# Optimization experiments

Hardware: AMD Instinct MI355X
Metric: run time of the kernel (lower is better)

## Reference

```python
import jax, jax.numpy as jnp
import numpy as np

DIM = 1024
HID = 2048
E = 8
K = 2
INV_SQRT2 = 1.0 / 1.41421356237


def setup_inputs() -> dict:
    key = jax.random.key(0)
    ks = jax.random.split(key, 10)
    s = lambda fan_in: 1.0 / np.sqrt(fan_in)
    return {
        "x": jax.random.normal(ks[0], (4, 2048, DIM), dtype=jnp.float32),
        "gate_w": jax.random.uniform(ks[1], (DIM, E), jnp.float32, -s(DIM), s(DIM)),
        "gate_b": jnp.zeros((E,), jnp.float32),
        "w1": jax.random.uniform(ks[2], (E, DIM, HID), jnp.float32, -s(DIM), s(DIM)),
        "b1": jnp.zeros((E, HID), jnp.float32),
        "w2": jax.random.uniform(ks[3], (E, DIM, HID), jnp.float32, -s(DIM), s(DIM)),
        "b2": jnp.zeros((E, HID), jnp.float32),
        "w3": jax.random.uniform(ks[4], (E, HID, DIM), jnp.float32, -s(HID), s(HID)),
        "b3": jnp.zeros((E, DIM), jnp.float32),
    }


def reference(x, gate_w, gate_b, w1, b1, w2, b2, w3, b3):
    # Gating
    logits = jnp.einsum("bsd,de->bse", x, gate_w) + gate_b          # [b,s,E]
    scores = jax.nn.softmax(logits, axis=-1)
    topk_scores, topk_idx = jax.lax.top_k(scores, K)                  # [b,s,K]

    # Load-balance (entropy) loss over mean expert usage
    usage = scores.mean(axis=(0, 1))                                   # [E]
    lb_loss = -(usage * jnp.log(usage + 1e-9)).sum()

    # Per-token combine weight for each expert: score if expert in top-k else 0
    onehot = jax.nn.one_hot(topk_idx, E, dtype=x.dtype)               # [b,s,K,E]
    comb = (topk_scores[..., None] * onehot).sum(axis=2)              # [b,s,E]

    # SwiGLU experts (batched over E via einsum)
    h = jnp.einsum("bsd,edh->ebsh", x, w1) + b1[:, None, None, :]
    g = jax.nn.silu(jnp.einsum("bsd,edh->ebsh", x, w2) + b2[:, None, None, :])
    eo = jnp.einsum("ebsh,ehd->ebsd", h * g, w3) + b3[:, None, None, :]
    eo = eo * INV_SQRT2

    # Weighted combine (zero weight where expert not selected)
    out = jnp.einsum("ebsd,bse->bsd", eo, comb)
    return out, lb_loss
```

## Files before the change

kernel.cpp:

```cpp
#include <hip/hip_runtime.h>
#include <cstdio>

#define NTOK 8192
#define DIM 1024
#define HID 2048
#define NE 8
#define NPAIR (NTOK * 2)

typedef __attribute__((ext_vector_type(8))) short bf16x8;
typedef __attribute__((ext_vector_type(4))) float f32x4;

typedef const __attribute__((address_space(1))) void* gas_ptr;
typedef __attribute__((address_space(3))) void* las_ptr;

__device__ __forceinline__ void async16(const void* g, void* s) {
  __builtin_amdgcn_global_load_lds((gas_ptr)g, (las_ptr)s, 16, 0, 0);
}

__device__ __forceinline__ unsigned short f2bf(float f) {
  unsigned int u = __float_as_uint(f);
  u = (u + 0x7fff + ((u >> 16) & 1)) >> 16;
  return (unsigned short)u;
}

__device__ __forceinline__ float bf2f(unsigned short u) {
  return __uint_as_float((unsigned int)u << 16);
}


#define S_BARRIER __builtin_amdgcn_s_barrier()
#define VM_WAIT(N) asm volatile("s_waitcnt vmcnt(" #N ")" ::: "memory")
#define LGKM0 asm volatile("s_waitcnt lgkmcnt(0)" ::: "memory")
#define CFENCE asm volatile("" ::: "memory")

__global__ __launch_bounds__(256) void prep_kernel(
    const float* __restrict__ w1, const float* __restrict__ w2,
    const float* __restrict__ w3, unsigned short* __restrict__ w1bt,
    unsigned short* __restrict__ w2bt, unsigned short* __restrict__ w3bt) {
  const int z = blockIdx.y;
  const int m = z >> 3, e = z & 7;
  int R, C;
  const float* in;
  unsigned short* outp;
  if (m == 0)      { R = DIM; C = HID; in = w1; outp = w1bt; }
  else if (m == 1) { R = DIM; C = HID; in = w2; outp = w2bt; }
  else             { R = HID; C = DIM; in = w3; outp = w3bt; }
  in += (size_t)e * DIM * HID;
  outp += (size_t)e * DIM * HID;

  const int tilesx = C >> 5;
  const int c0 = (blockIdx.x % tilesx) * 32;
  const int r0 = (blockIdx.x / tilesx) * 32;

  __shared__ float tile[32][33];
  const int c = threadIdx.x & 31, rr = threadIdx.x >> 5;
#pragma unroll
  for (int i = 0; i < 4; i++) {
    const int r = rr + i * 8;
    tile[r][c] = in[(size_t)(r0 + r) * C + c0 + c];
  }
  __syncthreads();
#pragma unroll
  for (int i = 0; i < 4; i++) {
    const int cc2 = rr + i * 8;
    outp[(size_t)(c0 + cc2) * R + r0 + c] = f2bf(tile[c][cc2]);
  }
}

__global__ __launch_bounds__(256) void gate_kernel(
    const float* __restrict__ x, const float* __restrict__ gw,
    const float* __restrict__ gb, unsigned short* __restrict__ xb,
    float* __restrict__ scores, int* __restrict__ route_e,
    float* __restrict__ route_w) {
  __shared__ float sgwT[NE][DIM];
  const int tid = threadIdx.x;
#pragma unroll
  for (int i = 0; i < 8; i++) {
    const int j = i * 256 + tid;
    const float4 v = ((const float4*)gw)[j];
    const int d = j >> 1, e0 = (j & 1) * 4;
    sgwT[e0 + 0][d] = v.x; sgwT[e0 + 1][d] = v.y;
    sgwT[e0 + 2][d] = v.z; sgwT[e0 + 3][d] = v.w;
  }
  __syncthreads();

  const int wv = tid >> 6, lane = tid & 63;
  const int t = blockIdx.x * 4 + wv;
  float acc[NE] = {0.f, 0.f, 0.f, 0.f, 0.f, 0.f, 0.f, 0.f};
  const float4* x4 = (const float4*)(x + (size_t)t * DIM);
#pragma unroll
  for (int i = 0; i < 4; i++) {
    const float4 xv = x4[i * 64 + lane];
    const int d4 = i * 64 + lane;
    ushort4 xbv;
    xbv.x = f2bf(xv.x); xbv.y = f2bf(xv.y);
    xbv.z = f2bf(xv.z); xbv.w = f2bf(xv.w);
    *(ushort4*)(xb + (size_t)t * DIM + d4 * 4) = xbv;
#pragma unroll
    for (int e = 0; e < NE; e++) {
      const float4 wv4 = *(const float4*)&sgwT[e][d4 * 4];
      acc[e] += xv.x * wv4.x + xv.y * wv4.y + xv.z * wv4.z + xv.w * wv4.w;
    }
  }
#pragma unroll
  for (int e = 0; e < NE; e++)
#pragma unroll
    for (int s = 32; s; s >>= 1) acc[e] += __shfl_xor(acc[e], s, 64);

  if (lane == 0) {
    float l[NE], m = -1e30f;
#pragma unroll
    for (int e = 0; e < NE; e++) { l[e] = acc[e] + gb[e]; m = fmaxf(m, l[e]); }
    float p[NE], sum = 0.f;
#pragma unroll
    for (int e = 0; e < NE; e++) { p[e] = __expf(l[e] - m); sum += p[e]; }
    const float inv = 1.f / sum;
    float s[NE];
#pragma unroll
    for (int e = 0; e < NE; e++) { s[e] = p[e] * inv; scores[t * NE + e] = s[e]; }
    int i1 = 0;
    for (int e = 1; e < NE; e++) if (s[e] > s[i1]) i1 = e;
    int i2 = -1;
    for (int e = 0; e < NE; e++) {
      if (e == i1) continue;
      if (i2 < 0 || s[e] > s[i2]) i2 = e;
    }
    route_e[t * 2] = i1; route_e[t * 2 + 1] = i2;
    route_w[t * 2] = s[i1]; route_w[t * 2 + 1] = s[i2];
  }
}

__global__ void finalize_kernel(const float* __restrict__ scores,
                                const int* __restrict__ route_e,
                                int* __restrict__ ctrl,
                                float* __restrict__ out_lb) {
  __shared__ float red[1024];
  __shared__ int hist[NE];
  const int tid = threadIdx.x;
  if (tid < NE) hist[tid] = 0;
  const int e = tid & 7, row = tid >> 3;
  float s = 0.f;
  for (int i = 0; i < 64; i++) s += scores[(size_t)(row + i * 128) * NE + e];
  red[tid] = s;
  __syncthreads();
#pragma unroll
  for (int i = 0; i < 16; i++)
    atomicAdd(&hist[route_e[i * 1024 + tid]], 1);
  for (int st = 512; st >= 8; st >>= 1) {
    __syncthreads();
    if (tid < st) red[tid] += red[tid + st];
  }
  __syncthreads();
  if (tid == 0) {
    float lb = 0.f;
    for (int ee = 0; ee < NE; ee++) {
      const float u = red[ee] * (1.f / 8192.f);
      lb -= u * __logf(u + 1e-9f);
    }
    *out_lb = lb;
    int o = 0;
    for (int ee = 0; ee < NE; ee++) {
      ctrl[ee] = hist[ee];
      ctrl[8 + ee] = o;
      ctrl[17 + ee] = o;
      o += hist[ee];
    }
    ctrl[16] = o;
  }
}

__global__ void scatter_kernel(const int* __restrict__ route_e,
                               const float* __restrict__ route_w,
                               int* __restrict__ ctrl,
                               int* __restrict__ tok_list,
                               float* __restrict__ pair_w,
                               int* __restrict__ pair_pos) {
  const int t = blockIdx.x * 256 + threadIdx.x;
  if (t >= NTOK) return;
#pragma unroll
  for (int k = 0; k < 2; k++) {
    const int e = route_e[t * 2 + k];
    const int p = atomicAdd(&ctrl[17 + e], 1);
    tok_list[p] = t;
    pair_w[p] = route_w[t * 2 + k] * 0.70710678118654752f;
    pair_pos[t * 2 + k] = p;
  }
}

__global__ __launch_bounds__(512) void stage1_kernel(
    const unsigned short* __restrict__ xb, const unsigned short* __restrict__ w1bt,
    const unsigned short* __restrict__ w2bt, const float* __restrict__ b1,
    const float* __restrict__ b2, const int* __restrict__ tok_list,
    const int* __restrict__ ctrl, unsigned short* __restrict__ act) {
  const int e = blockIdx.z;
  const int cnt = ctrl[e];
  const int ytile = blockIdx.y;
  if (ytile * 256 >= cnt) return;
  const int off = ctrl[8 + e];
  const int rows = min(256, cnt - ytile * 256);
  const int h0 = blockIdx.x * 128;

  __shared__ unsigned short sX[4][256 * 32];
  __shared__ unsigned short sW1[4][128 * 32];
  __shared__ unsigned short sW2[4][128 * 32];

  const int tid = threadIdx.x;
  const int wv = tid >> 6, lane = tid & 63;

  const int cl = ((tid & 3) ^ ((tid >> 3) & 3)) * 8;

  const unsigned short* w1p = w1bt + (size_t)e * HID * DIM + (size_t)h0 * DIM;
  const unsigned short* w2p = w2bt + (size_t)e * HID * DIM + (size_t)h0 * DIM;
  const unsigned short* gx0 =
      xb + (size_t)tok_list[off + ytile * 256 + min(tid >> 2, rows - 1)] * DIM + cl;
  const unsigned short* gx1 =
      xb + (size_t)tok_list[off + ytile * 256 + min(128 + (tid >> 2), rows - 1)] * DIM + cl;
  const unsigned short* gw1 = w1p + (size_t)(tid >> 2) * DIM + cl;
  const unsigned short* gw2 = w2p + (size_t)(tid >> 2) * DIM + cl;

  f32x4 ah[8][2], ag[8][2];
#pragma unroll
  for (int i = 0; i < 8; i++)
#pragma unroll
    for (int j = 0; j < 2; j++) {
      ah[i][j] = (f32x4){0.f, 0.f, 0.f, 0.f};
      ag[i][j] = (f32x4){0.f, 0.f, 0.f, 0.f};
    }

  const int wr = wv >> 2, wc = wv & 3;
  const int l15 = lane & 15, q = lane >> 4;
  const int pch = (q ^ ((l15 >> 1) & 3)) * 8;

#define S1_STAGE(B)                                   \
  do {                                                \
    async16(gx0, sX[B] + (wv * 64) * 8);              \
    async16(gx1, sX[B] + (512 + wv * 64) * 8);        \
    async16(gw1, sW1[B] + (wv * 64) * 8);             \
    async16(gw2, sW2[B] + (wv * 64) * 8);             \
    gx0 += 32; gx1 += 32; gw1 += 32; gw2 += 32;       \
  } while (0)

  S1_STAGE(0); S1_STAGE(1); S1_STAGE(2);
  VM_WAIT(8);
  S_BARRIER;
  CFENCE;

  const int NT = DIM / 32;
  for (int t = 0; t < NT; t++) {
    const int cur = t & 3;
    bf16x8 bx[8], a1[2], a2[2];
    {
      const unsigned short* xs = sX[cur];
      const unsigned short* w1s = sW1[cur];
      const unsigned short* w2s = sW2[cur];
#pragma unroll
      for (int i = 0; i < 8; i++)
        bx[i] = *(const bf16x8*)(xs + (wr * 128 + i * 16 + l15) * 32 + pch);
#pragma unroll
      for (int j = 0; j < 2; j++) {
        a1[j] = *(const bf16x8*)(w1s + (wc * 32 + j * 16 + l15) * 32 + pch);
        a2[j] = *(const bf16x8*)(w2s + (wc * 32 + j * 16 + l15) * 32 + pch);
      }
    }
    if (t < NT - 3) {
      const int nb = (t + 3) & 3;
      S1_STAGE(nb);
    }
    S_BARRIER;
    LGKM0;
    __builtin_amdgcn_sched_barrier(0);
    __builtin_amdgcn_s_setprio(1);
#pragma unroll
    for (int i = 0; i < 8; i++) {
      ah[i][0] = __builtin_amdgcn_mfma_f32_16x16x32_bf16(a1[0], bx[i], ah[i][0], 0, 0, 0);
      ag[i][0] = __builtin_amdgcn_mfma_f32_16x16x32_bf16(a2[0], bx[i], ag[i][0], 0, 0, 0);
      ah[i][1] = __builtin_amdgcn_mfma_f32_16x16x32_bf16(a1[1], bx[i], ah[i][1], 0, 0, 0);
      ag[i][1] = __builtin_amdgcn_mfma_f32_16x16x32_bf16(a2[1], bx[i], ag[i][1], 0, 0, 0);
    }
    __builtin_amdgcn_s_setprio(0);
    if (t < NT - 3) VM_WAIT(8);
    else if (t == NT - 3) VM_WAIT(4);
    else if (t == NT - 2) VM_WAIT(0);
    CFENCE;
    S_BARRIER;
  }
#undef S1_STAGE

  f32x4 b1v[2], b2v[2];
#pragma unroll
  for (int j = 0; j < 2; j++) {
    const int hc = h0 + wc * 32 + j * 16 + q * 4;
    b1v[j] = *(const f32x4*)(b1 + e * HID + hc);
    b2v[j] = *(const f32x4*)(b2 + e * HID + hc);
  }
#pragma unroll
  for (int i = 0; i < 8; i++) {
    const int trow = wr * 128 + i * 16 + l15;
    if (trow < rows) {
      const size_t gp = (size_t)(off + ytile * 256 + trow) * HID;
#pragma unroll
      for (int j = 0; j < 2; j++) {
        const int hc = h0 + wc * 32 + j * 16 + q * 4;
        ushort4 o;
        {
          const float hh = ah[i][j][0] + b1v[j][0];
          const float gg = ag[i][j][0] + b2v[j][0];
          o.x = f2bf(hh * (gg / (1.f + __expf(-gg))));
        }
        {
          const float hh = ah[i][j][1] + b1v[j][1];
          const float gg = ag[i][j][1] + b2v[j][1];
          o.y = f2bf(hh * (gg / (1.f + __expf(-gg))));
        }
        {
          const float hh = ah[i][j][2] + b1v[j][2];
          const float gg = ag[i][j][2] + b2v[j][2];
          o.z = f2bf(hh * (gg / (1.f + __expf(-gg))));
        }
        {
          const float hh = ah[i][j][3] + b1v[j][3];
          const float gg = ag[i][j][3] + b2v[j][3];
          o.w = f2bf(hh * (gg / (1.f + __expf(-gg))));
        }
        *(ushort4*)(act + gp + hc) = o;
      }
    }
  }
}

__global__ __launch_bounds__(512) void stage2s_kernel(
    const unsigned short* __restrict__ act, const unsigned short* __restrict__ w3bt,
    const float* __restrict__ b3, const float* __restrict__ pair_w,
    const int* __restrict__ ctrl, unsigned short* __restrict__ pair_out) {
  const int e = blockIdx.z;
  const int cnt = ctrl[e];
  const int ytile = blockIdx.y;
  if (ytile * 256 >= cnt) return;
  const int off = ctrl[8 + e];
  const int rows = min(256, cnt - ytile * 256);
  const int d0 = blockIdx.x * 256;
  const int rbase = off + ytile * 256;

  __shared__ unsigned short sA[4][256 * 32];
  __shared__ unsigned short sW[4][256 * 32];

  const int tid = threadIdx.x;
  const int wv = tid >> 6, lane = tid & 63;
  const int cl = ((tid & 3) ^ ((tid >> 3) & 3)) * 8;

  const unsigned short* w3p = w3bt + (size_t)e * DIM * HID + (size_t)d0 * HID;
  const unsigned short* ga0 =
      act + (size_t)(rbase + min(tid >> 2, rows - 1)) * HID + cl;
  const unsigned short* ga1 =
      act + (size_t)(rbase + min(128 + (tid >> 2), rows - 1)) * HID + cl;
  const unsigned short* gw0 = w3p + (size_t)(tid >> 2) * HID + cl;
  const unsigned short* gw1 = w3p + (size_t)(128 + (tid >> 2)) * HID + cl;

  f32x4 acc[8][4];
#pragma unroll
  for (int i = 0; i < 8; i++)
#pragma unroll
    for (int j = 0; j < 4; j++) acc[i][j] = (f32x4){0.f, 0.f, 0.f, 0.f};

  const int wr = wv >> 2, wc = wv & 3;
  const int l15 = lane & 15, q = lane >> 4;
  const int pch = (q ^ ((l15 >> 1) & 3)) * 8;

#define S2_STAGE(B)                                   \
  do {                                                \
    async16(ga0, sA[B] + (wv * 64) * 8);              \
    async16(ga1, sA[B] + (512 + wv * 64) * 8);        \
    async16(gw0, sW[B] + (wv * 64) * 8);              \
    async16(gw1, sW[B] + (512 + wv * 64) * 8);        \
    ga0 += 32; ga1 += 32; gw0 += 32; gw1 += 32;       \
  } while (0)

  S2_STAGE(0); S2_STAGE(1); S2_STAGE(2);
  VM_WAIT(8);
  S_BARRIER;
  CFENCE;

  const int NT = HID / 32;
  for (int t = 0; t < NT; t++) {
    const int cur = t & 3;
    bf16x8 af[8], bf[4];
    {
      const unsigned short* as = sA[cur];
      const unsigned short* ws = sW[cur];
#pragma unroll
      for (int i = 0; i < 8; i++)
        af[i] = *(const bf16x8*)(as + (wr * 128 + i * 16 + l15) * 32 + pch);
#pragma unroll
      for (int j = 0; j < 4; j++)
        bf[j] = *(const bf16x8*)(ws + (wc * 64 + j * 16 + l15) * 32 + pch);
    }
    if (t < NT - 3) {
      const int nb = (t + 3) & 3;
      S2_STAGE(nb);
    }
    S_BARRIER;
    LGKM0;
    __builtin_amdgcn_sched_barrier(0);
    __builtin_amdgcn_s_setprio(1);
#pragma unroll
    for (int i = 0; i < 8; i++)
#pragma unroll
      for (int j = 0; j < 4; j++)
        acc[i][j] =
            __builtin_amdgcn_mfma_f32_16x16x32_bf16(af[i], bf[j], acc[i][j], 0, 0, 0);
    __builtin_amdgcn_s_setprio(0);
    if (t < NT - 3) VM_WAIT(8);
    else if (t == NT - 3) VM_WAIT(4);
    else if (t == NT - 2) VM_WAIT(0);
    CFENCE;
    S_BARRIER;
  }
#undef S2_STAGE

#pragma unroll
  for (int i = 0; i < 8; i++)
#pragma unroll
    for (int rg = 0; rg < 4; rg++) {
      const int row = wr * 128 + i * 16 + q * 4 + rg;
      if (row < rows) {
        const int pr = rbase + row;
        const float wt = pair_w[pr];
#pragma unroll
        for (int j = 0; j < 4; j++) {
          const int dcol = d0 + wc * 64 + j * 16 + l15;
          pair_out[(size_t)pr * DIM + dcol] = f2bf((acc[i][j][rg] + b3[e * DIM + dcol]) * wt);
        }
      }
    }
}

__global__ __launch_bounds__(512) void stage2a_kernel(
    const unsigned short* __restrict__ act, const unsigned short* __restrict__ w3bt,
    const float* __restrict__ b3, const int* __restrict__ tok_list,
    const float* __restrict__ pair_w, const int* __restrict__ ctrl,
    float* __restrict__ out) {
  const int e = blockIdx.z;
  const int cnt = ctrl[e];
  const int ytile = blockIdx.y;
  if (ytile * 256 >= cnt) return;
  const int off = ctrl[8 + e];
  const int rows = min(256, cnt - ytile * 256);
  const int d0 = blockIdx.x * 256;
  const int rbase = off + ytile * 256;

  __shared__ unsigned short sA[4][256 * 32];
  __shared__ unsigned short sW[4][256 * 32];

  const int tid = threadIdx.x;
  const int wv = tid >> 6, lane = tid & 63;
  const int cl = ((tid & 3) ^ ((tid >> 3) & 3)) * 8;

  const unsigned short* w3p = w3bt + (size_t)e * DIM * HID + (size_t)d0 * HID;
  const unsigned short* ga0 =
      act + (size_t)(rbase + min(tid >> 2, rows - 1)) * HID + cl;
  const unsigned short* ga1 =
      act + (size_t)(rbase + min(128 + (tid >> 2), rows - 1)) * HID + cl;
  const unsigned short* gw0 = w3p + (size_t)(tid >> 2) * HID + cl;
  const unsigned short* gw1 = w3p + (size_t)(128 + (tid >> 2)) * HID + cl;

  f32x4 acc[8][4];
#pragma unroll
  for (int i = 0; i < 8; i++)
#pragma unroll
    for (int j = 0; j < 4; j++) acc[i][j] = (f32x4){0.f, 0.f, 0.f, 0.f};

  const int wr = wv >> 2, wc = wv & 3;
  const int l15 = lane & 15, q = lane >> 4;
  const int pch = (q ^ ((l15 >> 1) & 3)) * 8;

#define S2A_STAGE(B)                                  \
  do {                                                \
    async16(ga0, sA[B] + (wv * 64) * 8);              \
    async16(ga1, sA[B] + (512 + wv * 64) * 8);        \
    async16(gw0, sW[B] + (wv * 64) * 8);              \
    async16(gw1, sW[B] + (512 + wv * 64) * 8);        \
    ga0 += 32; ga1 += 32; gw0 += 32; gw1 += 32;       \
  } while (0)

  S2A_STAGE(0); S2A_STAGE(1); S2A_STAGE(2);
  VM_WAIT(8);
  S_BARRIER;
  CFENCE;

  const int NT = HID / 32;
  for (int t = 0; t < NT; t++) {
    const int cur = t & 3;
    bf16x8 af[8], bf[4];
    {
      const unsigned short* as = sA[cur];
      const unsigned short* ws = sW[cur];
#pragma unroll
      for (int i = 0; i < 8; i++)
        af[i] = *(const bf16x8*)(as + (wr * 128 + i * 16 + l15) * 32 + pch);
#pragma unroll
      for (int j = 0; j < 4; j++)
        bf[j] = *(const bf16x8*)(ws + (wc * 64 + j * 16 + l15) * 32 + pch);
    }
    if (t < NT - 3) {
      const int nb = (t + 3) & 3;
      S2A_STAGE(nb);
    }
    S_BARRIER;
    LGKM0;
    __builtin_amdgcn_sched_barrier(0);
    __builtin_amdgcn_s_setprio(1);
#pragma unroll
    for (int i = 0; i < 8; i++)
#pragma unroll
      for (int j = 0; j < 4; j++)
        acc[i][j] =
            __builtin_amdgcn_mfma_f32_16x16x32_bf16(af[i], bf[j], acc[i][j], 0, 0, 0);
    __builtin_amdgcn_s_setprio(0);
    if (t < NT - 3) VM_WAIT(8);
    else if (t == NT - 3) VM_WAIT(4);
    else if (t == NT - 2) VM_WAIT(0);
    CFENCE;
    S_BARRIER;
  }
#undef S2A_STAGE

#pragma unroll
  for (int i = 0; i < 8; i++)
#pragma unroll
    for (int rg = 0; rg < 4; rg++) {
      const int row = wr * 128 + i * 16 + q * 4 + rg;
      if (row < rows) {
        const int pr = rbase + row;
        const int tok = tok_list[pr];
        const float wt = pair_w[pr];
#pragma unroll
        for (int j = 0; j < 4; j++) {
          const int dcol = d0 + wc * 64 + j * 16 + l15;
          atomicAdd(out + (size_t)tok * DIM + dcol, (acc[i][j][rg] + b3[e * DIM + dcol]) * wt);
        }
      }
    }
}

__global__ __launch_bounds__(256) void combine_kernel(
    const unsigned short* __restrict__ pair_out, const int* __restrict__ pair_pos,
    float* __restrict__ out) {
  const int t = blockIdx.x;
  const int d = threadIdx.x * 4;
  const int p0 = pair_pos[t * 2], p1 = pair_pos[t * 2 + 1];
  const ushort4 a = *(const ushort4*)(pair_out + (size_t)p0 * DIM + d);
  const ushort4 b = *(const ushort4*)(pair_out + (size_t)p1 * DIM + d);
  float4 r;
  r.x = bf2f(a.x) + bf2f(b.x);
  r.y = bf2f(a.y) + bf2f(b.y);
  r.z = bf2f(a.z) + bf2f(b.z);
  r.w = bf2f(a.w) + bf2f(b.w);
  *(float4*)(out + (size_t)t * DIM + d) = r;
}

static const size_t SZ_XB  = (size_t)NTOK * DIM * 2;
static const size_t SZ_W   = (size_t)NE * DIM * HID * 2;
static const size_t SZ_ACT = (size_t)NPAIR * HID * 2;
static const size_t OFF_XB  = 0;
static const size_t OFF_W1  = OFF_XB + SZ_XB;
static const size_t OFF_W2  = OFF_W1 + SZ_W;
static const size_t OFF_W3  = OFF_W2 + SZ_W;
static const size_t OFF_ACT = OFF_W3 + SZ_W;
static const size_t OFF_SC  = OFF_ACT + SZ_ACT;
static const size_t OFF_RE  = OFF_SC + (size_t)NTOK * NE * 4;
static const size_t OFF_RW  = OFF_RE + (size_t)NPAIR * 4;
static const size_t OFF_TL  = OFF_RW + (size_t)NPAIR * 4;
static const size_t OFF_PW  = OFF_TL + (size_t)NPAIR * 4;
static const size_t OFF_PP  = OFF_PW + (size_t)NPAIR * 4;
static const size_t OFF_CT  = OFF_PP + (size_t)NPAIR * 4;
static const size_t WS_BASE = OFF_CT + 128;
static const size_t OFF_PO  = WS_BASE;
static const size_t WS_FULL = OFF_PO + (size_t)NPAIR * DIM * 2;

extern "C" void kernel_launch(void* const* d_in, const int* in_sizes, int n_in,
                              void* d_out, int out_size, void* d_ws, size_t ws_size,
                              hipStream_t stream) {
  const float* x      = (const float*)d_in[0];
  const float* gate_w = (const float*)d_in[1];
  const float* gate_b = (const float*)d_in[2];
  const float* w1     = (const float*)d_in[3];
  const float* b1     = (const float*)d_in[4];
  const float* w2     = (const float*)d_in[5];
  const float* b2     = (const float*)d_in[6];
  const float* w3     = (const float*)d_in[7];
  const float* b3     = (const float*)d_in[8];
  float* out = (float*)d_out;

  if (ws_size < WS_BASE) {
    fprintf(stderr, "kernel_launch: ws_size %zu < needed %zu\n", ws_size, WS_BASE);
    return;
  }
  const bool store_path = (ws_size >= WS_FULL);

  char* ws = (char*)d_ws;
  unsigned short* xb   = (unsigned short*)(ws + OFF_XB);
  unsigned short* w1bt = (unsigned short*)(ws + OFF_W1);
  unsigned short* w2bt = (unsigned short*)(ws + OFF_W2);
  unsigned short* w3bt = (unsigned short*)(ws + OFF_W3);
  unsigned short* act  = (unsigned short*)(ws + OFF_ACT);
  float* scores        = (float*)(ws + OFF_SC);
  int* route_e         = (int*)(ws + OFF_RE);
  float* route_w       = (float*)(ws + OFF_RW);
  int* tok_list        = (int*)(ws + OFF_TL);
  float* pair_w        = (float*)(ws + OFF_PW);
  int* pair_pos        = (int*)(ws + OFF_PP);
  int* ctrl            = (int*)(ws + OFF_CT);
  unsigned short* pout = (unsigned short*)(ws + OFF_PO);

  if (!store_path)
    hipMemsetAsync(d_out, 0, (size_t)out_size * sizeof(float), stream);

  prep_kernel<<<dim3(2048, 24), 256, 0, stream>>>(w1, w2, w3, w1bt, w2bt, w3bt);
  gate_kernel<<<2048, 256, 0, stream>>>(x, gate_w, gate_b, xb, scores, route_e,
                                        route_w);
  finalize_kernel<<<1, 1024, 0, stream>>>(scores, route_e, ctrl, out + (out_size - 1));
  scatter_kernel<<<32, 256, 0, stream>>>(route_e, route_w, ctrl, tok_list, pair_w,
                                         pair_pos);
  stage1_kernel<<<dim3(16, 32, 8), 512, 0, stream>>>(xb, w1bt, w2bt, b1, b2,
                                                     tok_list, ctrl, act);
  if (store_path) {
    stage2s_kernel<<<dim3(4, 32, 8), 512, 0, stream>>>(act, w3bt, b3, pair_w, ctrl, pout);
    combine_kernel<<<NTOK, 256, 0, stream>>>(pout, pair_pos, out);
  } else {
    stage2a_kernel<<<dim3(4, 32, 8), 512, 0, stream>>>(act, w3bt, b3, tok_list,
                                                       pair_w, ctrl, out);
  }
}
```

Measured before the change: 640.9 us.

## Vectorize weight transpose, batch scatter atomics, remap GEMM grids for XCD locality

The weight prep transpose now uses 64x64 tiles with float4 loads and ushort4 bf16 stores. The scatter kernel aggregates per-block expert counts in shared memory, so each block issues one global atomic per expert. The stage1 and stage2 GEMM launches become flat 1D grids whose block index is remapped so that blocks sharing an expert land on the same XCD (index mod 8), aiming to improve L2 reuse of expert weights. The trade-off is extra index arithmetic, and the scatter order within an expert now differs from before.

```diff
diff --git a/kernel.cpp b/kernel.cpp
--- a/kernel.cpp
+++ b/kernel.cpp
@@ -48,22 +48,34 @@
   in += (size_t)e * DIM * HID;
   outp += (size_t)e * DIM * HID;
 
-  const int tilesx = C >> 5;
-  const int c0 = (blockIdx.x % tilesx) * 32;
-  const int r0 = (blockIdx.x / tilesx) * 32;
-
-  __shared__ float tile[32][33];
-  const int c = threadIdx.x & 31, rr = threadIdx.x >> 5;
-#pragma unroll
-  for (int i = 0; i < 4; i++) {
-    const int r = rr + i * 8;
-    tile[r][c] = in[(size_t)(r0 + r) * C + c0 + c];
+  const int tilesx = C >> 6;
+  const int c0 = (blockIdx.x % tilesx) * 64;
+  const int r0 = (blockIdx.x / tilesx) * 64;
+
+  __shared__ float tT[64][65];
+  const int tid = threadIdx.x;
+  const int cq = tid & 15;
+  const int rr = tid >> 4;
+
+#pragma unroll
+  for (int p = 0; p < 4; p++) {
+    const int r = rr + p * 16;
+    const float4 v = *(const float4*)(in + (size_t)(r0 + r) * C + c0 + cq * 4);
+    tT[cq * 4 + 0][r] = v.x;
+    tT[cq * 4 + 1][r] = v.y;
+    tT[cq * 4 + 2][r] = v.z;
+    tT[cq * 4 + 3][r] = v.w;
   }
   __syncthreads();
 #pragma unroll
-  for (int i = 0; i < 4; i++) {
-    const int cc2 = rr + i * 8;
-    outp[(size_t)(c0 + cc2) * R + r0 + c] = f2bf(tile[c][cc2]);
+  for (int p = 0; p < 4; p++) {
+    const int cc = rr + p * 16;
+    ushort4 o;
+    o.x = f2bf(tT[cc][cq * 4 + 0]);
+    o.y = f2bf(tT[cc][cq * 4 + 1]);
+    o.z = f2bf(tT[cc][cq * 4 + 2]);
+    o.w = f2bf(tT[cc][cq * 4 + 3]);
+    *(ushort4*)(outp + (size_t)(c0 + cc) * R + r0 + cq * 4) = o;
   }
 }
 
@@ -169,22 +181,30 @@
   }
 }
 
-__global__ void scatter_kernel(const int* __restrict__ route_e,
-                               const float* __restrict__ route_w,
-                               int* __restrict__ ctrl,
-                               int* __restrict__ tok_list,
-                               float* __restrict__ pair_w,
-                               int* __restrict__ pair_pos) {
-  const int t = blockIdx.x * 256 + threadIdx.x;
-  if (t >= NTOK) return;
-#pragma unroll
-  for (int k = 0; k < 2; k++) {
-    const int e = route_e[t * 2 + k];
-    const int p = atomicAdd(&ctrl[17 + e], 1);
-    tok_list[p] = t;
-    pair_w[p] = route_w[t * 2 + k] * 0.70710678118654752f;
-    pair_pos[t * 2 + k] = p;
-  }
+__global__ __launch_bounds__(256) void scatter_kernel(
+    const int* __restrict__ route_e, const float* __restrict__ route_w,
+    int* __restrict__ ctrl, int* __restrict__ tok_list,
+    float* __restrict__ pair_w, int* __restrict__ pair_pos) {
+  __shared__ int lh[NE];
+  __shared__ int lbase[NE];
+  const int tid = threadIdx.x;
+  const int t = blockIdx.x * 256 + tid;
+  if (tid < NE) lh[tid] = 0;
+  __syncthreads();
+  const int e0 = route_e[t * 2], e1 = route_e[t * 2 + 1];
+  const int p0 = atomicAdd(&lh[e0], 1);
+  const int p1 = atomicAdd(&lh[e1], 1);
+  __syncthreads();
+  if (tid < NE) lbase[tid] = atomicAdd(&ctrl[17 + tid], lh[tid]);
+  __syncthreads();
+  const int q0 = lbase[e0] + p0;
+  const int q1 = lbase[e1] + p1;
+  tok_list[q0] = t;
+  pair_w[q0] = route_w[t * 2] * 0.70710678118654752f;
+  pair_pos[t * 2] = q0;
+  tok_list[q1] = t;
+  pair_w[q1] = route_w[t * 2 + 1] * 0.70710678118654752f;
+  pair_pos[t * 2 + 1] = q1;
 }
 
 __global__ __launch_bounds__(512) void stage1_kernel(
@@ -192,13 +212,16 @@
     const unsigned short* __restrict__ w2bt, const float* __restrict__ b1,
     const float* __restrict__ b2, const int* __restrict__ tok_list,
     const int* __restrict__ ctrl, unsigned short* __restrict__ act) {
-  const int e = blockIdx.z;
+  const int hbid = blockIdx.x;
+  const int lid = ((hbid & 7) << 9) + (hbid >> 3);
+  const int e = lid >> 9;
+  const int ytile = (lid >> 4) & 31;
+  const int h0 = (lid & 15) * 128;
+
   const int cnt = ctrl[e];
-  const int ytile = blockIdx.y;
   if (ytile * 256 >= cnt) return;
   const int off = ctrl[8 + e];
   const int rows = min(256, cnt - ytile * 256);
-  const int h0 = blockIdx.x * 128;
 
   __shared__ unsigned short sX[4][256 * 32];
   __shared__ unsigned short sW1[4][128 * 32];
@@ -332,13 +355,16 @@
     const unsigned short* __restrict__ act, const unsigned short* __restrict__ w3bt,
     const float* __restrict__ b3, const float* __restrict__ pair_w,
     const int* __restrict__ ctrl, unsigned short* __restrict__ pair_out) {
-  const int e = blockIdx.z;
+  const int hbid = blockIdx.x;
+  const int lid = ((hbid & 7) << 7) + (hbid >> 3);
+  const int e = lid >> 7;
+  const int ytile = (lid >> 2) & 31;
+  const int d0 = (lid & 3) * 256;
+
   const int cnt = ctrl[e];
-  const int ytile = blockIdx.y;
   if (ytile * 256 >= cnt) return;
   const int off = ctrl[8 + e];
   const int rows = min(256, cnt - ytile * 256);
-  const int d0 = blockIdx.x * 256;
   const int rbase = off + ytile * 256;
 
   __shared__ unsigned short sA[4][256 * 32];
@@ -439,13 +465,16 @@
     const float* __restrict__ b3, const int* __restrict__ tok_list,
     const float* __restrict__ pair_w, const int* __restrict__ ctrl,
     float* __restrict__ out) {
-  const int e = blockIdx.z;
+  const int hbid = blockIdx.x;
+  const int lid = ((hbid & 7) << 7) + (hbid >> 3);
+  const int e = lid >> 7;
+  const int ytile = (lid >> 2) & 31;
+  const int d0 = (lid & 3) * 256;
+
   const int cnt = ctrl[e];
-  const int ytile = blockIdx.y;
   if (ytile * 256 >= cnt) return;
   const int off = ctrl[8 + e];
   const int rows = min(256, cnt - ytile * 256);
-  const int d0 = blockIdx.x * 256;
   const int rbase = off + ytile * 256;
 
   __shared__ unsigned short sA[4][256 * 32];
@@ -615,19 +644,18 @@
   if (!store_path)
     hipMemsetAsync(d_out, 0, (size_t)out_size * sizeof(float), stream);
 
-  prep_kernel<<<dim3(2048, 24), 256, 0, stream>>>(w1, w2, w3, w1bt, w2bt, w3bt);
+  prep_kernel<<<dim3(512, 24), 256, 0, stream>>>(w1, w2, w3, w1bt, w2bt, w3bt);
   gate_kernel<<<2048, 256, 0, stream>>>(x, gate_w, gate_b, xb, scores, route_e,
                                         route_w);
   finalize_kernel<<<1, 1024, 0, stream>>>(scores, route_e, ctrl, out + (out_size - 1));
   scatter_kernel<<<32, 256, 0, stream>>>(route_e, route_w, ctrl, tok_list, pair_w,
                                          pair_pos);
-  stage1_kernel<<<dim3(16, 32, 8), 512, 0, stream>>>(xb, w1bt, w2bt, b1, b2,
-                                                     tok_list, ctrl, act);
+  stage1_kernel<<<4096, 512, 0, stream>>>(xb, w1bt, w2bt, b1, b2, tok_list, ctrl, act);
   if (store_path) {
-    stage2s_kernel<<<dim3(4, 32, 8), 512, 0, stream>>>(act, w3bt, b3, pair_w, ctrl, pout);
+    stage2s_kernel<<<1024, 512, 0, stream>>>(act, w3bt, b3, pair_w, ctrl, pout);
     combine_kernel<<<NTOK, 256, 0, stream>>>(pout, pair_pos, out);
   } else {
-    stage2a_kernel<<<dim3(4, 32, 8), 512, 0, stream>>>(act, w3bt, b3, tok_list,
-                                                       pair_w, ctrl, out);
-  }
-}
+    stage2a_kernel<<<1024, 512, 0, stream>>>(act, w3bt, b3, tok_list, pair_w,
+                                             ctrl, out);
+  }
+}
```

New measurement: 568.0 us. 11.4% less time.
